# Kernel optimization log

Hardware: AMD Instinct MI355X
Metric: run time of the kernel (lower is better)

## Reference

```python
import jax, jax.numpy as jnp
import numpy as np

T = 32768       # sequence length (batch=1 in original forward)
DY = 63         # mark dim; input_size = DY + 1 = 64
D_IN = 64
H = 256         # hidden_size
OUT = 32        # out_size
NI = 1024       # number of inducing points


def _lstm_scan(x, w_ih, w_hh, b_ih, b_hh, reverse):
    """Single-direction LSTM over [T, D] input, batch=1. PyTorch gate order i,f,g,o."""
    xg = x @ w_ih.T + (b_ih + b_hh)  # [T, 4H], input projection precomputed

    def step(carry, xg_t):
        h, c = carry
        g = xg_t + h @ w_hh.T
        i, f, gg, o = jnp.split(g, 4)
        c = jax.nn.sigmoid(f) * c + jax.nn.sigmoid(i) * jnp.tanh(gg)
        h = jax.nn.sigmoid(o) * jnp.tanh(c)
        return (h, c), h

    init = (jnp.zeros((H,), x.dtype), jnp.zeros((H,), x.dtype))
    _, hs = jax.lax.scan(step, init, xg, reverse=reverse)
    return hs  # [T, H]


def _bilstm(x, layer_params):
    for (wf, uf, bif, bhf, wb, ub, bib, bhb) in layer_params:
        hf = _lstm_scan(x, wf, uf, bif, bhf, False)
        hb = _lstm_scan(x, wb, ub, bib, bhb, True)
        x = jnp.concatenate([hf, hb], axis=-1)  # [T, 2H]
    return x


def setup_inputs() -> dict:
    key = jax.random.key(0)
    ks = iter(jax.random.split(key, 24))
    s = 1.0 / np.sqrt(H)  # PyTorch LSTM uniform(-1/sqrt(H), 1/sqrt(H)) init
    def U(shape):
        return jax.random.uniform(next(ks), shape, jnp.float32, -s, s)
    inp = {
        "Y": jax.random.normal(next(ks), (T, DY), jnp.float32),
        "dT": jax.random.uniform(next(ks), (T,), jnp.float32),
        "induce_idx": jnp.sort(jax.random.randint(next(ks), (NI,), 0, T)),
        # layer 0: input D_IN; layer 1: input 2H (bidirectional)
        "w_ih_l0f": U((4 * H, D_IN)), "w_hh_l0f": U((4 * H, H)), "b_ih_l0f": U((4 * H,)), "b_hh_l0f": U((4 * H,)),
        "w_ih_l0b": U((4 * H, D_IN)), "w_hh_l0b": U((4 * H, H)), "b_ih_l0b": U((4 * H,)), "b_hh_l0b": U((4 * H,)),
        "w_ih_l1f": U((4 * H, 2 * H)), "w_hh_l1f": U((4 * H, H)), "b_ih_l1f": U((4 * H,)), "b_hh_l1f": U((4 * H,)),
        "w_ih_l1b": U((4 * H, 2 * H)), "w_hh_l1b": U((4 * H, H)), "b_ih_l1b": U((4 * H,)), "b_hh_l1b": U((4 * H,)),
        "fc_weight": jax.random.normal(next(ks), (2 * H, 2 * OUT), jnp.float32),
    }
    return inp


def reference(Y, dT, induce_idx,
              w_ih_l0f, w_hh_l0f, b_ih_l0f, b_hh_l0f,
              w_ih_l0b, w_hh_l0b, b_ih_l0b, b_hh_l0b,
              w_ih_l1f, w_hh_l1f, b_ih_l1f, b_hh_l1f,
              w_ih_l1b, w_hh_l1b, b_ih_l1b, b_hh_l1b,
              fc_weight):
    x = jnp.concatenate([Y, dT[:, None]], axis=1)  # [T, D_IN]
    layer_params = [
        (w_ih_l0f, w_hh_l0f, b_ih_l0f, b_hh_l0f, w_ih_l0b, w_hh_l0b, b_ih_l0b, b_hh_l0b),
        (w_ih_l1f, w_hh_l1f, b_ih_l1f, b_hh_l1f, w_ih_l1b, w_hh_l1b, b_ih_l1b, b_hh_l1b),
    ]
    h = _bilstm(x, layer_params)          # [T, 2H]
    out = h @ fc_weight                    # [T, 2*OUT]
    sel = out[induce_idx]                  # [NI, 2*OUT]
    return sel[:, :OUT], sel[:, OUT:]
```

## Files before the change

### kernel.cpp

```cpp
#include <hip/hip_runtime.h>

typedef unsigned int u32;
typedef unsigned short u16;
typedef _Float16 f16;
typedef _Float16 f16x2 __attribute__((ext_vector_type(2)));
typedef _Float16 f16x4 __attribute__((ext_vector_type(4)));

#define T_SEQ 32768

static const size_t OFF_DT   = 0;
static const size_t OFF_FLG  = 1024;
static const size_t OFF_MAP  = 4096;
static const size_t OFF_H1G  = 135168;
static const size_t OFF_BIAS = 1183744;
static const size_t OFF_FCW  = 1200128;
static const size_t OFF_WQ8  = 1331200;
static const size_t OFF_WIH0 = 3428352;
static const size_t OFF_WIH1 = 3690496;
static const size_t OFF_XQ   = 5787648;
static const size_t OFF_H0   = 9981952;
static const size_t OFF_XG   = 43536384;
static const size_t XG_DIR   = (size_t)T_SEQ * 1024 * 2;
static const size_t NEED_PAR = OFF_XG + 2 * XG_DIR;

__device__ __forceinline__ float bf2f(u16 u) {
  union { u32 i; float f; } v; v.i = ((u32)u) << 16; return v.f;
}
__device__ __forceinline__ u16 f2bf(float f) {
  union { float f; u32 i; } v; v.f = f;
  u32 u = v.i;
  return (u16)((u + 0x7fffu + ((u >> 16) & 1u)) >> 16);
}
__device__ __forceinline__ u32 packf2(float a, float b) {
  f16x2 p; p.x = (f16)a; p.y = (f16)b;
  return __builtin_bit_cast(u32, p);
}
__device__ __forceinline__ u32 bf2f2(u32 v) {
  union { u32 i; float f; } lo, hi;
  lo.i = v << 16; hi.i = v & 0xffff0000u;
  return packf2(lo.f, hi.f);
}
__device__ __forceinline__ float ldf(const void* p, size_t i, u32 isf) {
  return isf ? ((const float*)p)[i] : bf2f(((const u16*)p)[i]);
}
__device__ __forceinline__ float fdot2f(f16x2 a, f16x2 b, float c) {
#if __has_builtin(__builtin_amdgcn_fdot2)
  return __builtin_amdgcn_fdot2(a, b, c, false);
#else
  return c + (float)a.x * (float)b.x + (float)a.y * (float)b.y;
#endif
}
__device__ __forceinline__ float fdotu(u32 a, u32 b, float c) {
  return fdot2f(__builtin_bit_cast(f16x2, a), __builtin_bit_cast(f16x2, b), c);
}
__device__ __forceinline__ int sdot4(u32 a, u32 b, int c) {
#if __has_builtin(__builtin_amdgcn_sdot4)
  return __builtin_amdgcn_sdot4((int)a, (int)b, c, false);
#else
  int r = c;
#pragma unroll
  for (int j = 0; j < 4; ++j)
    r += (int)(signed char)(a >> (8 * j)) * (int)(signed char)(b >> (8 * j));
  return r;
#endif
}
__device__ __forceinline__ int dpp_xor1(int x) {
#if __has_builtin(__builtin_amdgcn_update_dpp)
  return __builtin_amdgcn_update_dpp(0, x, 0xB1, 0xF, 0xF, true);
#else
  return __shfl_xor(x, 1);
#endif
}
__device__ __forceinline__ int dpp_xor2(int x) {
#if __has_builtin(__builtin_amdgcn_update_dpp)
  return __builtin_amdgcn_update_dpp(0, x, 0x4E, 0xF, 0xF, true);
#else
  return __shfl_xor(x, 2);
#endif
}
__device__ __forceinline__ int dpp_ror8(int x) {
#if __has_builtin(__builtin_amdgcn_update_dpp)
  return __builtin_amdgcn_update_dpp(0, x, 0x128, 0xF, 0xF, true);
#else
  return __shfl_xor(x, 8);
#endif
}
template <int CTRL>
__device__ __forceinline__ float dpp_bcastf(float x) {
#if __has_builtin(__builtin_amdgcn_update_dpp)
  return __builtin_bit_cast(float,
      __builtin_amdgcn_update_dpp(0, __builtin_bit_cast(int, x), CTRL, 0xF, 0xF, true));
#else
  return __shfl(x, (threadIdx.x & ~3) + (CTRL & 3));
#endif
}
__device__ __forceinline__ float tanhf_fast(float x) {
  return 1.0f - 2.0f * __builtin_amdgcn_rcpf(1.0f + __builtin_amdgcn_exp2f(2.8853900817779268f * x));
}
__device__ __forceinline__ void wg_barrier_lds() {
  asm volatile("s_waitcnt lgkmcnt(0)" ::: "memory");
  __builtin_amdgcn_s_barrier();
  asm volatile("" ::: "memory");
}

__global__ void k_detect(const u16* __restrict__ probe, u32* __restrict__ dt) {
  __shared__ int cnt;
  if (threadIdx.x == 0) cnt = 0;
  __syncthreads();
  int bad = 0;
  for (int i = threadIdx.x; i < 8192; i += 256) {
    float v = bf2f(probe[i]);
    if (!(v * v <= 16.0f)) bad++;
  }
  atomicAdd(&cnt, bad);
  __syncthreads();
  if (threadIdx.x == 0) *dt = (cnt > 64) ? 1u : 0u;
}

__global__ void k_conv_pairs(const void* __restrict__ src, u32* __restrict__ dst,
                             int np, const u32* __restrict__ dtp) {
  u32 isf = *dtp;
  int i = blockIdx.x * 256 + threadIdx.x;
  if (i >= np) return;
  if (isf) {
    const float* s = (const float*)src;
    dst[i] = packf2(s[2 * i], s[2 * i + 1]);
  } else {
    dst[i] = bf2f2(((const u32*)src)[i]);
  }
}

__global__ void k_quant(const void* __restrict__ src, u32* __restrict__ dst,
                        const u32* __restrict__ dtp) {
  u32 isf = *dtp;
  int i = blockIdx.x * 256 + threadIdx.x;
  int row = i >> 6, c = i & 63;
  u32 out = 0;
#pragma unroll
  for (int j = 0; j < 4; ++j) {
    float w = ldf(src, (size_t)row * 256 + 4 * c + j, isf);
    int q = (int)rintf(w * 2048.0f);
    q = q > 127 ? 127 : (q < -127 ? -127 : q);
    out |= ((u32)(q & 0xff)) << (8 * j);
  }
  dst[i] = out;
}

__global__ void k_conv_misc(const void* bi0f, const void* bh0f, const void* bi0b, const void* bh0b,
                            const void* bi1f, const void* bh1f, const void* bi1b, const void* bh1b,
                            const void* fcb, float* __restrict__ bias, float* __restrict__ fcw,
                            u32* __restrict__ flags, int* __restrict__ map,
                            const u32* __restrict__ dtp) {
  u32 isf = *dtp;
  int i = blockIdx.x * 256 + threadIdx.x;
  if (i < 4096) {
    int ld = i >> 10, r = i & 1023;
    const void* bi; const void* bh;
    if (ld == 0)      { bi = bi0f; bh = bh0f; }
    else if (ld == 1) { bi = bi0b; bh = bh0b; }
    else if (ld == 2) { bi = bi1f; bh = bh1f; }
    else              { bi = bi1b; bh = bh1b; }
    bias[i] = ldf(bi, r, isf) + ldf(bh, r, isf);
  } else if (i < 36864) {
    fcw[i - 4096] = ldf(fcb, i - 4096, isf);
  } else if (i < 36992) {
    flags[i - 36864] = 0;
  } else if (i < 69760) {
    map[i - 36992] = -1;
  }
}

__global__ void k_conv_x(const void* __restrict__ Y, const void* __restrict__ dT,
                         u32* __restrict__ xq, const u32* __restrict__ dtp) {
  u32 isf = *dtp;
  int i = blockIdx.x * 256 + threadIdx.x;
  if (i >= T_SEQ * 32) return;
  int t = i >> 5, m = i & 31, k2 = 2 * m;
  float a = ldf(Y, (size_t)t * 63 + k2, isf);
  float b = (k2 + 1 < 63) ? ldf(Y, (size_t)t * 63 + k2 + 1, isf) : ldf(dT, t, isf);
  xq[i] = packf2(a, b);
}

__global__ void k_map_set(const int* __restrict__ idx, int* __restrict__ map) {
  int i = blockIdx.x * 256 + threadIdx.x;
  if (i < 1024) map[idx[i]] = i;
}

__global__ __launch_bounds__(256) void k_gemm(
    const u32* __restrict__ Aq, const u32* __restrict__ Wc,
    const float* __restrict__ bias, f16* __restrict__ xgT, int Kp, int rev) {
  int t0 = blockIdx.x << 6, r0 = blockIdx.y << 6;
  int tid = threadIdx.x, tx = tid & 15, ty = tid >> 4;
  __shared__ u32 As[64][33];
  __shared__ u32 Bs[64][33];
  float acc[4][4] = {};
  for (int kp0 = 0; kp0 < Kp; kp0 += 32) {
#pragma unroll
    for (int i = 0; i < 8; ++i) {
      int idx = tid + (i << 8);
      int row = idx >> 5, kp = idx & 31, kpg = kp0 + kp;
      As[row][kp] = Aq[(size_t)(t0 + row) * Kp + kpg];
      Bs[row][kp] = Wc[(size_t)(r0 + row) * Kp + kpg];
    }
    __syncthreads();
#pragma unroll 4
    for (int kk = 0; kk < 32; ++kk) {
      u32 av[4], bv[4];
#pragma unroll
      for (int i = 0; i < 4; ++i) av[i] = As[ty * 4 + i][kk];
#pragma unroll
      for (int i = 0; i < 4; ++i) bv[i] = Bs[tx * 4 + i][kk];
#pragma unroll
      for (int i = 0; i < 4; ++i)
#pragma unroll
        for (int j = 0; j < 4; ++j)
          acc[i][j] = fdotu(av[i], bv[j], acc[i][j]);
    }
    __syncthreads();
  }
  int tb = t0 + (ty << 2);
#pragma unroll
  for (int j = 0; j < 4; ++j) {
    int rr = r0 + tx * 4 + j;
    float b = bias[rr];
    f16 v0 = (f16)(acc[0][j] + b);
    f16 v1 = (f16)(acc[1][j] + b);
    f16 v2 = (f16)(acc[2][j] + b);
    f16 v3 = (f16)(acc[3][j] + b);
    size_t base = (size_t)rr * T_SEQ;
    f16x4 v;
    size_t pos;
    if (rev) { pos = base + (size_t)(T_SEQ - 4 - tb); v = (f16x4){v3, v2, v1, v0}; }
    else     { pos = base + (size_t)tb;               v = (f16x4){v0, v1, v2, v3}; }
    *(f16x4*)(xgT + pos) = v;
  }
}

template <bool HASMAP>
__global__ __launch_bounds__(1024, 4) void k_recur2(
    const f16* __restrict__ xgT, const u32* __restrict__ wq,
    f16* __restrict__ h_full, f16* __restrict__ h1g,
    const int* __restrict__ map, int dir0) {
  const int dir = dir0 + blockIdx.x;
  const int tid = threadIdx.x;
  const int l = tid & 63, wv = tid >> 6;
  const int r16 = l >> 4, gbit = (l >> 2) & 1;
  const int s = (l & 3) | ((l >> 1) & 4);
  const int ubase = (wv << 4) + (r16 << 2) + (gbit << 1);
  const int u_own = ubase + (s >> 2);
  const u32* wqd = wq + ((size_t)dir << 16);

  __shared__ __align__(16) unsigned char hb8[2][256];

  uint4 w[16];
  {
    const uint4* pw = (const uint4*)wqd;
#pragma unroll
    for (int t = 0; t < 8; ++t) {
      int rho = t ^ s;
      int R = ((rho & 3) << 8) | (ubase + (rho >> 2));
      w[2 * t]     = pw[(size_t)R * 16 + 2 * s];
      w[2 * t + 1] = pw[(size_t)R * 16 + 2 * s + 1];
    }
  }

  if (tid < 128) ((u32*)hb8)[tid] = 0;

  const float ksc = 1.0f / (2048.0f * 127.0f);
  const float sk = ((s & 3) == 2) ? 2.8853900817779268f : -1.4426950408889634f;
  const float aa = ((s & 3) == 2) ? -2.0f : 1.0f;
  const float bb = ((s & 3) == 2) ? 1.0f : 0.0f;
  const float kk = sk * ksc;

  const f16* xg_d = xgT + (size_t)blockIdx.x * ((size_t)T_SEQ * 1024);
  const f16* xrow = xg_d + (size_t)(((s & 3) << 8) | u_own) * T_SEQ;

  const int tstep = dir ? -1 : 1;
  int t = dir ? (T_SEQ - 1) : 0;
  int mp = HASMAP ? map[t] : -1;
  float c_state = 0.f;

  f16* hout = h_full ? (h_full + (size_t)t * 512 + (dir << 8) + u_own) : nullptr;
  const ptrdiff_t hstride = (ptrdiff_t)tstep * 512;

  uint4 xcur = *(const uint4*)xrow;
  uint4 xnxt = xcur;

  __syncthreads();

  for (int ch = 0; ch < T_SEQ / 8; ++ch) {
    if (ch + 1 < T_SEQ / 8) xnxt = *(const uint4*)(xrow + (((size_t)ch + 1) << 3));
#pragma unroll
    for (int j = 0; j < 8; ++j) {
      u32 dw = (j >> 1) == 0 ? xcur.x : (j >> 1) == 1 ? xcur.y
             : (j >> 1) == 2 ? xcur.z : xcur.w;
      f16x2 pr = __builtin_bit_cast(f16x2, dw);
      float xbs = sk * (float)((j & 1) ? pr.y : pr.x);

      int ms = mp;
      if (HASMAP) {
        int tn = t + tstep;
        int idx2 = ((unsigned)tn < T_SEQ) ? tn : t;
        mp = map[idx2];
      }

      const uint4* hp = (const uint4*)hb8 + ((j & 1) << 4) + (s << 1);
      uint4 hv0 = hp[0], hv1 = hp[1];

      int a0, a1, a2, a3, a4, a5, a6, a7;
#define DOTSLOT(A, T)                                             \
      A = sdot4(w[2*T+1].w, hv1.w,                                \
          sdot4(w[2*T+1].z, hv1.z,                                \
          sdot4(w[2*T+1].y, hv1.y,                                \
          sdot4(w[2*T+1].x, hv1.x,                                \
          sdot4(w[2*T].w,   hv0.w,                                \
          sdot4(w[2*T].z,   hv0.z,                                \
          sdot4(w[2*T].y,   hv0.y,                                \
          sdot4(w[2*T].x,   hv0.x, 0))))))));
      DOTSLOT(a0, 0) DOTSLOT(a1, 1) DOTSLOT(a2, 2) DOTSLOT(a3, 3)
      DOTSLOT(a4, 4) DOTSLOT(a5, 5) DOTSLOT(a6, 6) DOTSLOT(a7, 7)
#undef DOTSLOT
      int b0 = a0 + dpp_xor1(a1);
      int b1 = a2 + dpp_xor1(a3);
      int b2 = a4 + dpp_xor1(a5);
      int b3 = a6 + dpp_xor1(a7);
      int c0 = b0 + dpp_xor2(b1);
      int c1 = b2 + dpp_xor2(b3);
      int e  = c0 + dpp_ror8(c1);

      float xarg = __builtin_fmaf((float)e, kk, xbs);
      float r = __builtin_amdgcn_rcpf(1.0f + __builtin_amdgcn_exp2f(xarg));
      float g = __builtin_fmaf(aa, r, bb);
      float gi = dpp_bcastf<0x00>(g);
      float gf = dpp_bcastf<0x55>(g);
      float gg = dpp_bcastf<0xAA>(g);
      float go = dpp_bcastf<0xFF>(g);
      c_state = __builtin_fmaf(gf, c_state, gi * gg);
      float h = go * tanhf_fast(c_state);
      int q8 = (int)rintf(h * 127.0f);
      if ((l & 3) == 0) {
        hb8[(j & 1) ^ 1][u_own] = (unsigned char)(q8 & 0xff);
        if (h_full) *hout = (f16)h;
        if (HASMAP && ms >= 0) h1g[(size_t)ms * 512 + (dir << 8) + u_own] = (f16)h;
      }
      wg_barrier_lds();
      t += tstep;
      hout += hstride;
    }
    xcur = xnxt;
  }
}

__global__ void k_fc(const f16* __restrict__ hbase, const int* __restrict__ mapn,
                     const int* __restrict__ idx, const float* __restrict__ fcw,
                     void* __restrict__ out, const u32* __restrict__ dtp) {
  u32 isf = *dtp;
  int n = blockIdx.x;
  int cc = threadIdx.x;
  int slot = mapn ? mapn[idx[n]] : idx[n];
  const f16* hp = hbase + (size_t)slot * 512;
  float acc = 0.f;
#pragma unroll 8
  for (int k = 0; k < 512; ++k) acc += (float)hp[k] * fcw[k * 64 + cc];
  int o = (cc < 32) ? (n * 32 + cc) : (32 * 1024 + n * 32 + (cc - 32));
  if (isf) ((float*)out)[o] = acc;
  else     ((u16*)out)[o]   = f2bf(acc);
}

extern "C" void kernel_launch(void* const* d_in, const int* in_sizes, int n_in,
                              void* d_out, int out_size, void* d_ws, size_t ws_size,
                              hipStream_t stream) {
  const void* Y        = d_in[0];
  const void* dT       = d_in[1];
  const int*  idx      = (const int*)d_in[2];
  const void* w_ih_l0f = d_in[3];
  const void* w_hh_l0f = d_in[4];
  const void* b_ih_l0f = d_in[5];
  const void* b_hh_l0f = d_in[6];
  const void* w_ih_l0b = d_in[7];
  const void* w_hh_l0b = d_in[8];
  const void* b_ih_l0b = d_in[9];
  const void* b_hh_l0b = d_in[10];
  const void* w_ih_l1f = d_in[11];
  const void* w_hh_l1f = d_in[12];
  const void* b_ih_l1f = d_in[13];
  const void* b_hh_l1f = d_in[14];
  const void* w_ih_l1b = d_in[15];
  const void* w_hh_l1b = d_in[16];
  const void* b_ih_l1b = d_in[17];
  const void* b_hh_l1b = d_in[18];
  const void* fcbf     = d_in[19];

  char* ws = (char*)d_ws;
  u32*  dt    = (u32*)(ws + OFF_DT);
  u32*  flags = (u32*)(ws + OFF_FLG);
  int*  map   = (int*)(ws + OFF_MAP);
  f16*  h1g   = (f16*)(ws + OFF_H1G);
  float* bias = (float*)(ws + OFF_BIAS);
  float* fcw  = (float*)(ws + OFF_FCW);
  u32*  wq8   = (u32*)(ws + OFF_WQ8);
  u32*  wih0  = (u32*)(ws + OFF_WIH0);
  u32*  wih1  = (u32*)(ws + OFF_WIH1);
  u32*  xq    = (u32*)(ws + OFF_XQ);
  f16*  h0    = (f16*)(ws + OFF_H0);
  f16*  xg    = (f16*)(ws + OFF_XG);
  f16*  xg1   = xg + XG_DIR / 2;

  const int par = (ws_size >= NEED_PAR) ? 1 : 0;

  k_detect<<<1, 256, 0, stream>>>((const u16*)w_hh_l0f, dt);
  k_quant<<<256, 256, 0, stream>>>(w_hh_l0f, wq8 + 0 * 65536, dt);
  k_quant<<<256, 256, 0, stream>>>(w_hh_l0b, wq8 + 1 * 65536, dt);
  k_quant<<<256, 256, 0, stream>>>(w_hh_l1f, wq8 + 2 * 65536, dt);
  k_quant<<<256, 256, 0, stream>>>(w_hh_l1b, wq8 + 3 * 65536, dt);
  k_conv_pairs<<<128, 256, 0, stream>>>(w_ih_l0f, wih0 + 0, 32768, dt);
  k_conv_pairs<<<128, 256, 0, stream>>>(w_ih_l0b, wih0 + 32768, 32768, dt);
  k_conv_pairs<<<1024, 256, 0, stream>>>(w_ih_l1f, wih1 + 0, 262144, dt);
  k_conv_pairs<<<1024, 256, 0, stream>>>(w_ih_l1b, wih1 + 262144, 262144, dt);
  k_conv_misc<<<273, 256, 0, stream>>>(b_ih_l0f, b_hh_l0f, b_ih_l0b, b_hh_l0b,
                                       b_ih_l1f, b_hh_l1f, b_ih_l1b, b_hh_l1b,
                                       fcbf, bias, fcw, flags, map, dt);
  k_conv_x<<<4096, 256, 0, stream>>>(Y, dT, xq, dt);
  k_map_set<<<4, 256, 0, stream>>>(idx, map);

  dim3 ggrid(T_SEQ / 64, 16);
  if (par) {
    k_gemm<<<ggrid, 256, 0, stream>>>(xq, wih0, bias, xg, 32, 0);
    k_gemm<<<ggrid, 256, 0, stream>>>(xq, wih0 + 32768, bias + 1024, xg1, 32, 1);
    k_recur2<false><<<2, 1024, 0, stream>>>(xg, wq8, h0, nullptr, nullptr, 0);
    k_gemm<<<ggrid, 256, 0, stream>>>((const u32*)h0, wih1, bias + 2048, xg, 256, 0);
    k_gemm<<<ggrid, 256, 0, stream>>>((const u32*)h0, wih1 + 262144, bias + 3072, xg1, 256, 1);
    k_recur2<false><<<2, 1024, 0, stream>>>(xg, wq8 + 2 * 65536, h0, nullptr, nullptr, 0);
    k_fc<<<1024, 64, 0, stream>>>(h0, nullptr, idx, fcw, d_out, dt);
  } else {
    k_gemm<<<ggrid, 256, 0, stream>>>(xq, wih0, bias, xg, 32, 0);
    k_recur2<false><<<1, 1024, 0, stream>>>(xg, wq8, h0, nullptr, nullptr, 0);
    k_gemm<<<ggrid, 256, 0, stream>>>(xq, wih0 + 32768, bias + 1024, xg, 32, 1);
    k_recur2<false><<<1, 1024, 0, stream>>>(xg, wq8, h0, nullptr, nullptr, 1);
    k_gemm<<<ggrid, 256, 0, stream>>>((const u32*)h0, wih1, bias + 2048, xg, 256, 0);
    k_recur2<true><<<1, 1024, 0, stream>>>(xg, wq8 + 2 * 65536, nullptr, h1g, map, 0);
    k_gemm<<<ggrid, 256, 0, stream>>>((const u32*)h0, wih1 + 262144, bias + 3072, xg, 256, 1);
    k_recur2<true><<<1, 1024, 0, stream>>>(xg, wq8 + 2 * 65536, nullptr, h1g, map, 1);
    k_fc<<<1024, 64, 0, stream>>>(h1g, map, idx, fcw, d_out, dt);
  }
}
```

Baseline: 61.07 ms.

## Halve recurrent workgroup to 512 threads with two hidden units per lane

The LSTM recurrence kernel now runs 8 waves instead of 16, and each lane computes two hidden units (A and B) with twice the register-resident int8 weights. This reduces the number of waves taking part in the per-timestep workgroup barrier, which dominates the serial scan. The trade-off is doubled per-lane dot-product and activation work plus higher register pressure (32 uint4 weight registers), which could lengthen the per-step critical path.

```diff
diff --git a/kernel.cpp b/kernel.cpp
--- a/kernel.cpp
+++ b/kernel.cpp
@@ -237,7 +237,7 @@
 }
 
 template <bool HASMAP>
-__global__ __launch_bounds__(1024, 4) void k_recur2(
+__global__ __launch_bounds__(512, 2) void k_recur2(
     const f16* __restrict__ xgT, const u32* __restrict__ wq,
     f16* __restrict__ h_full, f16* __restrict__ h1g,
     const int* __restrict__ map, int dir0) {
@@ -246,21 +246,25 @@
   const int l = tid & 63, wv = tid >> 6;
   const int r16 = l >> 4, gbit = (l >> 2) & 1;
   const int s = (l & 3) | ((l >> 1) & 4);
-  const int ubase = (wv << 4) + (r16 << 2) + (gbit << 1);
-  const int u_own = ubase + (s >> 2);
+  const int ubase = (((wv << 3) | (r16 << 1) | gbit) << 2);
+  const int uA = ubase + (s >> 2);
+  const int uB = uA + 2;
   const u32* wqd = wq + ((size_t)dir << 16);
 
   __shared__ __align__(16) unsigned char hb8[2][256];
 
-  uint4 w[16];
+  uint4 wA[16], wB[16];
   {
     const uint4* pw = (const uint4*)wqd;
 #pragma unroll
     for (int t = 0; t < 8; ++t) {
       int rho = t ^ s;
-      int R = ((rho & 3) << 8) | (ubase + (rho >> 2));
-      w[2 * t]     = pw[(size_t)R * 16 + 2 * s];
-      w[2 * t + 1] = pw[(size_t)R * 16 + 2 * s + 1];
+      int RA = ((rho & 3) << 8) | (ubase + (rho >> 2));
+      int RB = ((rho & 3) << 8) | (ubase + 2 + (rho >> 2));
+      wA[2 * t]     = pw[(size_t)RA * 16 + 2 * s];
+      wA[2 * t + 1] = pw[(size_t)RA * 16 + 2 * s + 1];
+      wB[2 * t]     = pw[(size_t)RB * 16 + 2 * s];
+      wB[2 * t + 1] = pw[(size_t)RB * 16 + 2 * s + 1];
     }
   }
 
@@ -273,29 +277,38 @@
   const float kk = sk * ksc;
 
   const f16* xg_d = xgT + (size_t)blockIdx.x * ((size_t)T_SEQ * 1024);
-  const f16* xrow = xg_d + (size_t)(((s & 3) << 8) | u_own) * T_SEQ;
+  const f16* xrowA = xg_d + (size_t)(((s & 3) << 8) | uA) * T_SEQ;
+  const f16* xrowB = xg_d + (size_t)(((s & 3) << 8) | uB) * T_SEQ;
 
   const int tstep = dir ? -1 : 1;
   int t = dir ? (T_SEQ - 1) : 0;
   int mp = HASMAP ? map[t] : -1;
-  float c_state = 0.f;
-
-  f16* hout = h_full ? (h_full + (size_t)t * 512 + (dir << 8) + u_own) : nullptr;
+  float cA = 0.f, cB = 0.f;
+
+  f16* hout = h_full ? (h_full + (size_t)t * 512 + (dir << 8) + uA) : nullptr;
   const ptrdiff_t hstride = (ptrdiff_t)tstep * 512;
 
-  uint4 xcur = *(const uint4*)xrow;
-  uint4 xnxt = xcur;
+  uint4 xcurA = *(const uint4*)xrowA;
+  uint4 xcurB = *(const uint4*)xrowB;
+  uint4 xnxtA = xcurA, xnxtB = xcurB;
 
   __syncthreads();
 
   for (int ch = 0; ch < T_SEQ / 8; ++ch) {
-    if (ch + 1 < T_SEQ / 8) xnxt = *(const uint4*)(xrow + (((size_t)ch + 1) << 3));
+    if (ch + 1 < T_SEQ / 8) {
+      xnxtA = *(const uint4*)(xrowA + (((size_t)ch + 1) << 3));
+      xnxtB = *(const uint4*)(xrowB + (((size_t)ch + 1) << 3));
+    }
 #pragma unroll
     for (int j = 0; j < 8; ++j) {
-      u32 dw = (j >> 1) == 0 ? xcur.x : (j >> 1) == 1 ? xcur.y
-             : (j >> 1) == 2 ? xcur.z : xcur.w;
-      f16x2 pr = __builtin_bit_cast(f16x2, dw);
-      float xbs = sk * (float)((j & 1) ? pr.y : pr.x);
+      u32 dwA = (j >> 1) == 0 ? xcurA.x : (j >> 1) == 1 ? xcurA.y
+              : (j >> 1) == 2 ? xcurA.z : xcurA.w;
+      u32 dwB = (j >> 1) == 0 ? xcurB.x : (j >> 1) == 1 ? xcurB.y
+              : (j >> 1) == 2 ? xcurB.z : xcurB.w;
+      f16x2 prA = __builtin_bit_cast(f16x2, dwA);
+      f16x2 prB = __builtin_bit_cast(f16x2, dwB);
+      float xbsA = sk * (float)((j & 1) ? prA.y : prA.x);
+      float xbsB = sk * (float)((j & 1) ? prB.y : prB.x);
 
       int ms = mp;
       if (HASMAP) {
@@ -308,46 +321,72 @@
       uint4 hv0 = hp[0], hv1 = hp[1];
 
       int a0, a1, a2, a3, a4, a5, a6, a7;
-#define DOTSLOT(A, T)                                             \
-      A = sdot4(w[2*T+1].w, hv1.w,                                \
-          sdot4(w[2*T+1].z, hv1.z,                                \
-          sdot4(w[2*T+1].y, hv1.y,                                \
-          sdot4(w[2*T+1].x, hv1.x,                                \
-          sdot4(w[2*T].w,   hv0.w,                                \
-          sdot4(w[2*T].z,   hv0.z,                                \
-          sdot4(w[2*T].y,   hv0.y,                                \
-          sdot4(w[2*T].x,   hv0.x, 0))))))));
-      DOTSLOT(a0, 0) DOTSLOT(a1, 1) DOTSLOT(a2, 2) DOTSLOT(a3, 3)
-      DOTSLOT(a4, 4) DOTSLOT(a5, 5) DOTSLOT(a6, 6) DOTSLOT(a7, 7)
+      int g0, g1, g2, g3, g4, g5, g6, g7;
+#define DOTSLOT(A, W, T)                                          \
+      A = sdot4(W[2*T+1].w, hv1.w,                                \
+          sdot4(W[2*T+1].z, hv1.z,                                \
+          sdot4(W[2*T+1].y, hv1.y,                                \
+          sdot4(W[2*T+1].x, hv1.x,                                \
+          sdot4(W[2*T].w,   hv0.w,                                \
+          sdot4(W[2*T].z,   hv0.z,                                \
+          sdot4(W[2*T].y,   hv0.y,                                \
+          sdot4(W[2*T].x,   hv0.x, 0))))))));
+      DOTSLOT(a0, wA, 0) DOTSLOT(a1, wA, 1) DOTSLOT(a2, wA, 2) DOTSLOT(a3, wA, 3)
+      DOTSLOT(a4, wA, 4) DOTSLOT(a5, wA, 5) DOTSLOT(a6, wA, 6) DOTSLOT(a7, wA, 7)
+      DOTSLOT(g0, wB, 0) DOTSLOT(g1, wB, 1) DOTSLOT(g2, wB, 2) DOTSLOT(g3, wB, 3)
+      DOTSLOT(g4, wB, 4) DOTSLOT(g5, wB, 5) DOTSLOT(g6, wB, 6) DOTSLOT(g7, wB, 7)
 #undef DOTSLOT
-      int b0 = a0 + dpp_xor1(a1);
-      int b1 = a2 + dpp_xor1(a3);
-      int b2 = a4 + dpp_xor1(a5);
-      int b3 = a6 + dpp_xor1(a7);
-      int c0 = b0 + dpp_xor2(b1);
-      int c1 = b2 + dpp_xor2(b3);
-      int e  = c0 + dpp_ror8(c1);
-
-      float xarg = __builtin_fmaf((float)e, kk, xbs);
-      float r = __builtin_amdgcn_rcpf(1.0f + __builtin_amdgcn_exp2f(xarg));
-      float g = __builtin_fmaf(aa, r, bb);
-      float gi = dpp_bcastf<0x00>(g);
-      float gf = dpp_bcastf<0x55>(g);
-      float gg = dpp_bcastf<0xAA>(g);
-      float go = dpp_bcastf<0xFF>(g);
-      c_state = __builtin_fmaf(gf, c_state, gi * gg);
-      float h = go * tanhf_fast(c_state);
-      int q8 = (int)rintf(h * 127.0f);
+      int bA0 = a0 + dpp_xor1(a1);
+      int bA1 = a2 + dpp_xor1(a3);
+      int bA2 = a4 + dpp_xor1(a5);
+      int bA3 = a6 + dpp_xor1(a7);
+      int cA0 = bA0 + dpp_xor2(bA1);
+      int cA1 = bA2 + dpp_xor2(bA3);
+      int eA  = cA0 + dpp_ror8(cA1);
+      int bB0 = g0 + dpp_xor1(g1);
+      int bB1 = g2 + dpp_xor1(g3);
+      int bB2 = g4 + dpp_xor1(g5);
+      int bB3 = g6 + dpp_xor1(g7);
+      int cB0 = bB0 + dpp_xor2(bB1);
+      int cB1 = bB2 + dpp_xor2(bB3);
+      int eB  = cB0 + dpp_ror8(cB1);
+
+      float xargA = __builtin_fmaf((float)eA, kk, xbsA);
+      float rA = __builtin_amdgcn_rcpf(1.0f + __builtin_amdgcn_exp2f(xargA));
+      float gA = __builtin_fmaf(aa, rA, bb);
+      float giA = dpp_bcastf<0x00>(gA);
+      float gfA = dpp_bcastf<0x55>(gA);
+      float ggA = dpp_bcastf<0xAA>(gA);
+      float goA = dpp_bcastf<0xFF>(gA);
+      cA = __builtin_fmaf(gfA, cA, giA * ggA);
+      float hA = goA * tanhf_fast(cA);
+      int qA = (int)rintf(hA * 127.0f);
+      float xargB = __builtin_fmaf((float)eB, kk, xbsB);
+      float rB = __builtin_amdgcn_rcpf(1.0f + __builtin_amdgcn_exp2f(xargB));
+      float gB = __builtin_fmaf(aa, rB, bb);
+      float giB = dpp_bcastf<0x00>(gB);
+      float gfB = dpp_bcastf<0x55>(gB);
+      float ggB = dpp_bcastf<0xAA>(gB);
+      float goB = dpp_bcastf<0xFF>(gB);
+      cB = __builtin_fmaf(gfB, cB, giB * ggB);
+      float hB = goB * tanhf_fast(cB);
+      int qB = (int)rintf(hB * 127.0f);
+
       if ((l & 3) == 0) {
-        hb8[(j & 1) ^ 1][u_own] = (unsigned char)(q8 & 0xff);
-        if (h_full) *hout = (f16)h;
-        if (HASMAP && ms >= 0) h1g[(size_t)ms * 512 + (dir << 8) + u_own] = (f16)h;
+        hb8[(j & 1) ^ 1][uA] = (unsigned char)(qA & 0xff);
+        hb8[(j & 1) ^ 1][uB] = (unsigned char)(qB & 0xff);
+        if (h_full) { hout[0] = (f16)hA; hout[2] = (f16)hB; }
+        if (HASMAP && ms >= 0) {
+          f16* hg = h1g + (size_t)ms * 512 + (dir << 8) + uA;
+          hg[0] = (f16)hA; hg[2] = (f16)hB;
+        }
       }
       wg_barrier_lds();
       t += tstep;
       hout += hstride;
     }
-    xcur = xnxt;
+    xcurA = xnxtA;
+    xcurB = xnxtB;
   }
 }
 
@@ -427,20 +466,20 @@
   if (par) {
     k_gemm<<<ggrid, 256, 0, stream>>>(xq, wih0, bias, xg, 32, 0);
     k_gemm<<<ggrid, 256, 0, stream>>>(xq, wih0 + 32768, bias + 1024, xg1, 32, 1);
-    k_recur2<false><<<2, 1024, 0, stream>>>(xg, wq8, h0, nullptr, nullptr, 0);
+    k_recur2<false><<<2, 512, 0, stream>>>(xg, wq8, h0, nullptr, nullptr, 0);
     k_gemm<<<ggrid, 256, 0, stream>>>((const u32*)h0, wih1, bias + 2048, xg, 256, 0);
     k_gemm<<<ggrid, 256, 0, stream>>>((const u32*)h0, wih1 + 262144, bias + 3072, xg1, 256, 1);
-    k_recur2<false><<<2, 1024, 0, stream>>>(xg, wq8 + 2 * 65536, h0, nullptr, nullptr, 0);
+    k_recur2<false><<<2, 512, 0, stream>>>(xg, wq8 + 2 * 65536, h0, nullptr, nullptr, 0);
     k_fc<<<1024, 64, 0, stream>>>(h0, nullptr, idx, fcw, d_out, dt);
   } else {
     k_gemm<<<ggrid, 256, 0, stream>>>(xq, wih0, bias, xg, 32, 0);
-    k_recur2<false><<<1, 1024, 0, stream>>>(xg, wq8, h0, nullptr, nullptr, 0);
+    k_recur2<false><<<1, 512, 0, stream>>>(xg, wq8, h0, nullptr, nullptr, 0);
     k_gemm<<<ggrid, 256, 0, stream>>>(xq, wih0 + 32768, bias + 1024, xg, 32, 1);
-    k_recur2<false><<<1, 1024, 0, stream>>>(xg, wq8, h0, nullptr, nullptr, 1);
+    k_recur2<false><<<1, 512, 0, stream>>>(xg, wq8, h0, nullptr, nullptr, 1);
     k_gemm<<<ggrid, 256, 0, stream>>>((const u32*)h0, wih1, bias + 2048, xg, 256, 0);
-    k_recur2<true><<<1, 1024, 0, stream>>>(xg, wq8 + 2 * 65536, nullptr, h1g, map, 0);
+    k_recur2<true><<<1, 512, 0, stream>>>(xg, wq8 + 2 * 65536, nullptr, h1g, map, 0);
     k_gemm<<<ggrid, 256, 0, stream>>>((const u32*)h0, wih1 + 262144, bias + 3072, xg, 256, 1);
-    k_recur2<true><<<1, 1024, 0, stream>>>(xg, wq8 + 2 * 65536, nullptr, h1g, map, 1);
+    k_recur2<true><<<1, 512, 0, stream>>>(xg, wq8 + 2 * 65536, nullptr, h1g, map, 1);
     k_fc<<<1024, 64, 0, stream>>>(h1g, map, idx, fcw, d_out, dt);
   }
 }
```

Result: faster. 55.99 ms (-8.3%).
